# Performance work log

Hardware: AMD Instinct MI355X
Metric: run time of the kernel (lower is better)

The kernel has to match this reference:

```python
import jax, jax.numpy as jnp
import numpy as np

N_WORDS = 256
N_BOOKS = 8
L_WORD = 32
GUMBEL_TEMP = 0.5
EPS_LOG = 1e-9
EPS_GUMBEL = 1e-20


def setup_inputs() -> dict:
    key = jax.random.key(0)
    k1, k2 = jax.random.split(key)
    X = jax.random.normal(k1, (32768, N_BOOKS * L_WORD), dtype=jnp.float32)
    C = jax.random.normal(k2, (N_WORDS, N_BOOKS * L_WORD), dtype=jnp.float32)
    return {"X": X, "C": C}


def reference(X, C):
    N = X.shape[0]
    # (N, B, L) and (M, B, L) per-book views
    x = X.reshape(N, N_BOOKS, L_WORD)
    c = C.reshape(N_WORDS, N_BOOKS, L_WORD)

    xc = jnp.einsum('nbl,mbl->bnm', x, c)            # (B, N, M)
    x2 = jnp.sum(x * x, axis=-1).T[:, :, None]       # (B, N, 1)
    c2 = jnp.sum(c * c, axis=-1).T[:, None, :]       # (B, 1, M)
    logits = 2.0 * xc - x2 - c2                      # (B, N, M)

    # gumbel_softmax sampling path (hard=False): softmax -> log -> +gumbel -> softmax/temp
    p = jax.nn.softmax(logits, axis=-1)
    logp = jnp.log(p + EPS_LOG)
    u = jax.random.uniform(jax.random.key(42), logp.shape, dtype=logp.dtype)
    g = -jnp.log(-jnp.log(u + EPS_GUMBEL) + EPS_GUMBEL)
    soft_prob = jax.nn.softmax((logp + g) / GUMBEL_TEMP, axis=-1)  # (B, N, M)

    # per-book codebook matmul, concatenated along feature dim
    Q = jnp.einsum('bnm,mbl->nbl', soft_prob, c).reshape(N, N_BOOKS * L_WORD)
    return (Q, soft_prob)
```

## Files before the change

kernel.cpp:

```cpp
#include <hip/hip_runtime.h>
#include <stdint.h>

#define NROWS 32768
#define NMQ   (NROWS * 256)
#define QSIZE (NROWS * 256)

typedef __attribute__((ext_vector_type(8))) short short8;
typedef __attribute__((ext_vector_type(4))) float f32x4;

#define LOG2E 1.4426950408889634f

__device__ __forceinline__ uint32_t tfp32(uint32_t idx) {
    const uint32_t K1 = 42u;
    const uint32_t K2 = 0x1BD11BDAu ^ 42u;
    uint32_t x0 = 0u;
    uint32_t x1 = idx + K1;
#define TFR(r) { x0 += x1; x1 = __builtin_rotateleft32(x1, (r)) ^ x0; }
    TFR(13) TFR(15) TFR(26) TFR(6)
    x0 += K1; x1 += K2 + 1u;
    TFR(17) TFR(29) TFR(16) TFR(24)
    x0 += K2; x1 += 2u;
    TFR(13) TFR(15) TFR(26) TFR(6)
    x1 += K1 + 3u;
    TFR(17) TFR(29) TFR(16) TFR(24)
    x0 += K1; x1 += K2 + 4u;
    TFR(13) TFR(15) TFR(26) TFR(6)
    x0 += K2; x1 += 5u;
#undef TFR
    return x0 ^ x1;
}

__device__ __forceinline__ float u01f(uint32_t b) {
    return __uint_as_float((b >> 9) | 0x3F800000u) - 1.0f;
}

__device__ __forceinline__ void split8(const float* p, short8& h, short8& l) {
#pragma unroll
    for (int e = 0; e < 8; ++e) {
        float f = p[e];
        uint32_t ib = __float_as_uint(f);
        h[e] = (short)(ib >> 16);
        float fh = __uint_as_float(ib & 0xFFFF0000u);
        l[e] = (short)(__float_as_uint(f - fh) >> 16);
    }
}

__device__ __forceinline__ unsigned short bf16rne(float f) {
    uint32_t ib = __float_as_uint(f);
    uint32_t r = ib + 0x7FFFu + ((ib >> 16) & 1u);
    return (unsigned short)(r >> 16);
}

#define DPPX(x, ctrl) \
    __int_as_float(__builtin_amdgcn_update_dpp(__float_as_int(x), \
        __float_as_int(x), (ctrl), 0xf, 0xf, false))

__device__ __forceinline__ float red16_max(float x) {
    x = fmaxf(x, DPPX(x, 0xB1));
    x = fmaxf(x, DPPX(x, 0x4E));
    x = fmaxf(x, DPPX(x, 0x141));
    x = fmaxf(x, DPPX(x, 0x140));
    return x;
}
__device__ __forceinline__ float red16_sum(float x) {
    x += DPPX(x, 0xB1);
    x += DPPX(x, 0x4E);
    x += DPPX(x, 0x141);
    x += DPPX(x, 0x140);
    return x;
}

__global__ __launch_bounds__(512)
void pq_fused(const float* __restrict__ X, const float* __restrict__ C,
              float* __restrict__ out)
{
    __shared__ short8 CBH[16 * 64];
    __shared__ short8 CBL[16 * 64];
    __shared__ short8 CQB[16 * 64];
    __shared__ __align__(16) unsigned short PL[8][16][256];
    __shared__ float  C2T[256];

    const int t    = threadIdx.x;
    const int wv   = t >> 6;
    const int lane = t & 63;
    const int g    = lane >> 4;
    const int c    = lane & 15;
    const int b      = blockIdx.x & 7;
    const int rowblk = blockIdx.x >> 3;

    for (int i = t; i < 1024; i += 512) {
        const int tile = i >> 6, l = i & 63;
        const int m = tile * 16 + (l & 15);
        const int kb = (l >> 4) * 8;
        const float* cp = C + (size_t)m * 256 + b * 32 + kb;
        float buf[8];
        *reinterpret_cast<float4*>(&buf[0]) = *reinterpret_cast<const float4*>(cp);
        *reinterpret_cast<float4*>(&buf[4]) = *reinterpret_cast<const float4*>(cp + 4);
        short8 h, lo;
        split8(buf, h, lo);
        CBH[i] = h;
        CBL[i] = lo;
    }
    for (int i = t; i < 1024; i += 512) {
        const int ch = i >> 7, lt = (i >> 6) & 1, l = i & 63;
        const int gg = l >> 4, cc = l & 15;
        short8 v;
#pragma unroll
        for (int e = 0; e < 8; ++e)
            v[e] = (short)bf16rne(C[(size_t)(ch * 32 + gg * 8 + e) * 256 + b * 32 + lt * 16 + cc]);
        CQB[i] = v;
    }
    if (t < 256) {
        const float* cp = C + (size_t)t * 256 + b * 32;
        float s = 0.f;
#pragma unroll
        for (int q = 0; q < 8; ++q) {
            float4 v = *reinterpret_cast<const float4*>(cp + q * 4);
            s = fmaf(v.x, v.x, fmaf(v.y, v.y, fmaf(v.z, v.z, fmaf(v.w, v.w, s))));
        }
        C2T[t] = s;
    }
    __syncthreads();

    float bias[16];
#pragma unroll
    for (int tt = 0; tt < 16; ++tt)
        bias[tt] = -2.0f * LOG2E * C2T[tt * 16 + c];

    float* __restrict__ Qout = out;
    float* __restrict__ SP   = out + QSIZE;

    for (int it = 0; it < 2; ++it) {
        const int r0 = (rowblk << 8) + (it << 7) + (wv << 4);

        short8 xh, xl;
        {
            const float* xp = X + (size_t)(r0 + c) * 256 + b * 32 + g * 8;
            float buf[8];
            *reinterpret_cast<float4*>(&buf[0]) = *reinterpret_cast<const float4*>(xp);
            *reinterpret_cast<float4*>(&buf[4]) = *reinterpret_cast<const float4*>(xp + 4);
            split8(buf, xh, xl);
        }

        f32x4 acc[16];
#pragma unroll
        for (int tt = 0; tt < 16; ++tt) {
            short8 bh = CBH[tt * 64 + lane];
            short8 bl = CBL[tt * 64 + lane];
            f32x4 a = {0.f, 0.f, 0.f, 0.f};
            a = __builtin_amdgcn_mfma_f32_16x16x32_bf16(xh, bh, a, 0, 0, 0);
            a = __builtin_amdgcn_mfma_f32_16x16x32_bf16(xl, bh, a, 0, 0, 0);
            a = __builtin_amdgcn_mfma_f32_16x16x32_bf16(xh, bl, a, 0, 0, 0);
            acc[tt] = a;
        }

#define PROCJ(jj)                                                               \
        {                                                                       \
            const int n = r0 + g * 4 + (jj);                                    \
            const uint32_t base = (uint32_t)b * (uint32_t)NMQ                   \
                                + (uint32_t)n * 256u + (uint32_t)c;             \
            float z[16];                                                        \
            float mx = -3.4e38f;                                                \
            _Pragma("unroll")                                                   \
            for (int tt = 0; tt < 16; ++tt) {                                   \
                uint32_t rb = tfp32(base + (uint32_t)(tt * 16));                \
                float u  = u01f(rb);                                            \
                float tg = -__log2f(u + 1e-20f);                                \
                float lt2 = __log2f(tg);                                        \
                float zz = fmaf(acc[tt][(jj)], 4.0f * LOG2E, bias[tt])          \
                         - 2.0f * lt2;                                          \
                z[tt] = zz;                                                     \
                mx = fmaxf(mx, zz);                                             \
            }                                                                   \
            mx = red16_max(mx);                                                 \
            float s = 0.f;                                                      \
            _Pragma("unroll")                                                   \
            for (int tt = 0; tt < 16; ++tt) {                                   \
                float e = __builtin_amdgcn_exp2f(z[tt] - mx);                   \
                z[tt] = e;                                                      \
                s += e;                                                         \
            }                                                                   \
            s = red16_sum(s);                                                   \
            const float rs = __builtin_amdgcn_rcpf(s);                          \
            float* spg = SP + (size_t)b * NMQ + (size_t)n * 256 + c;            \
            unsigned short* plrow = &PL[wv][g * 4 + (jj)][0];                   \
            _Pragma("unroll")                                                   \
            for (int tt = 0; tt < 16; ++tt) {                                   \
                float p = z[tt] * rs;                                           \
                __builtin_nontemporal_store(p, spg + tt * 16);                  \
                plrow[((tt ^ g) << 4) + c] =                                    \
                    (unsigned short)(__float_as_uint(p) >> 16);                 \
            }                                                                   \
        }
        PROCJ(0) PROCJ(1) PROCJ(2) PROCJ(3)
#undef PROCJ

        {
            f32x4 q0 = {0.f, 0.f, 0.f, 0.f};
            f32x4 q1 = {0.f, 0.f, 0.f, 0.f};
#pragma unroll
            for (int ch = 0; ch < 8; ++ch) {
                const int ttp = (2 * ch + (g >> 1)) ^ (c >> 2);
                const short8 pa = *reinterpret_cast<const short8*>(
                    &PL[wv][c][ttp * 16 + (g & 1) * 8]);
                q0 = __builtin_amdgcn_mfma_f32_16x16x32_bf16(pa, CQB[(ch * 2 + 0) * 64 + lane], q0, 0, 0, 0);
                q1 = __builtin_amdgcn_mfma_f32_16x16x32_bf16(pa, CQB[(ch * 2 + 1) * 64 + lane], q1, 0, 0, 0);
            }
#pragma unroll
            for (int j2 = 0; j2 < 4; ++j2) {
                float* qp = Qout + (size_t)(r0 + g * 4 + j2) * 256 + b * 32 + c;
                __builtin_nontemporal_store(q0[j2], qp);
                __builtin_nontemporal_store(q1[j2], qp + 16);
            }
        }
    }
}

extern "C" void kernel_launch(void* const* d_in, const int* in_sizes, int n_in,
                              void* d_out, int out_size, void* d_ws, size_t ws_size,
                              hipStream_t stream) {
    const float* X = (const float*)d_in[0];
    const float* C = (const float*)d_in[1];
    float* out = (float*)d_out;

    dim3 grid(1024);
    dim3 block(512);
    hipLaunchKernelGGL(pq_fused, grid, block, 0, stream, X, C, out);
}
```

Baseline: 188.4 us.

## Halve probability LDS staging buffer and split Q matmul into two chunks

The per-wave bf16 probability staging buffer shrinks from 16 to 8 rows by running the Q MFMA after every two row-groups instead of once after all four. The C2T scratch array now aliases that buffer, with an extra barrier after the bias load. Launch bounds request 4 blocks per SM so more blocks fit in LDS and registers at once, for better latency hiding. In exchange the Q MFMAs run twice as often, with half the lanes storing redundant rows masked out, so MFMA work doubles.

```diff
diff --git a/kernel.cpp b/kernel.cpp
--- a/kernel.cpp
+++ b/kernel.cpp
@@ -70,15 +70,15 @@
     return x;
 }
 
-__global__ __launch_bounds__(512)
+__global__ __launch_bounds__(512, 4)
 void pq_fused(const float* __restrict__ X, const float* __restrict__ C,
               float* __restrict__ out)
 {
     __shared__ short8 CBH[16 * 64];
     __shared__ short8 CBL[16 * 64];
     __shared__ short8 CQB[16 * 64];
-    __shared__ __align__(16) unsigned short PL[8][16][256];
-    __shared__ float  C2T[256];
+    __shared__ __align__(16) unsigned short PL[8][8][256];
+    float* C2T = reinterpret_cast<float*>(&PL[0][0][0]);
 
     const int t    = threadIdx.x;
     const int wv   = t >> 6;
@@ -126,6 +126,7 @@
 #pragma unroll
     for (int tt = 0; tt < 16; ++tt)
         bias[tt] = -2.0f * LOG2E * C2T[tt * 16 + c];
+    __syncthreads();
 
     float* __restrict__ Qout = out;
     float* __restrict__ SP   = out + QSIZE;
@@ -183,7 +184,7 @@
             s = red16_sum(s);                                                   \
             const float rs = __builtin_amdgcn_rcpf(s);                          \
             float* spg = SP + (size_t)b * NMQ + (size_t)n * 256 + c;            \
-            unsigned short* plrow = &PL[wv][g * 4 + (jj)][0];                   \
+            unsigned short* plrow = &PL[wv][g * 2 + ((jj) & 1)][0];             \
             _Pragma("unroll")                                                   \
             for (int tt = 0; tt < 16; ++tt) {                                   \
                 float p = z[tt] * rs;                                           \
@@ -192,27 +193,37 @@
                     (unsigned short)(__float_as_uint(p) >> 16);                 \
             }                                                                   \
         }
-        PROCJ(0) PROCJ(1) PROCJ(2) PROCJ(3)
+
+#define QCHUNK(joff)                                                            \
+        {                                                                       \
+            f32x4 q0 = {0.f, 0.f, 0.f, 0.f};                                    \
+            f32x4 q1 = {0.f, 0.f, 0.f, 0.f};                                    \
+            _Pragma("unroll")                                                   \
+            for (int ch = 0; ch < 8; ++ch) {                                    \
+                const int ttp = (ch * 2 + (g >> 1)) ^ ((c & 7) >> 1);           \
+                const short8 pa = *reinterpret_cast<const short8*>(             \
+                    &PL[wv][c & 7][ttp * 16 + (g & 1) * 8]);                    \
+                q0 = __builtin_amdgcn_mfma_f32_16x16x32_bf16(                   \
+                         pa, CQB[(ch * 2 + 0) * 64 + lane], q0, 0, 0, 0);       \
+                q1 = __builtin_amdgcn_mfma_f32_16x16x32_bf16(                   \
+                         pa, CQB[(ch * 2 + 1) * 64 + lane], q1, 0, 0, 0);       \
+            }                                                                   \
+            if (g < 2) {                                                        \
+                _Pragma("unroll")                                               \
+                for (int reg = 0; reg < 4; ++reg) {                             \
+                    const int rl = g * 4 + reg;                                 \
+                    const int n = r0 + ((rl >> 1) << 2) + (rl & 1) + (joff);    \
+                    float* qp = Qout + (size_t)n * 256 + b * 32 + c;            \
+                    __builtin_nontemporal_store(q0[reg], qp);                   \
+                    __builtin_nontemporal_store(q1[reg], qp + 16);              \
+                }                                                               \
+            }                                                                   \
+        }
+
+        PROCJ(0) PROCJ(1) QCHUNK(0)
+        PROCJ(2) PROCJ(3) QCHUNK(2)
 #undef PROCJ
-
-        {
-            f32x4 q0 = {0.f, 0.f, 0.f, 0.f};
-            f32x4 q1 = {0.f, 0.f, 0.f, 0.f};
-#pragma unroll
-            for (int ch = 0; ch < 8; ++ch) {
-                const int ttp = (2 * ch + (g >> 1)) ^ (c >> 2);
-                const short8 pa = *reinterpret_cast<const short8*>(
-                    &PL[wv][c][ttp * 16 + (g & 1) * 8]);
-                q0 = __builtin_amdgcn_mfma_f32_16x16x32_bf16(pa, CQB[(ch * 2 + 0) * 64 + lane], q0, 0, 0, 0);
-                q1 = __builtin_amdgcn_mfma_f32_16x16x32_bf16(pa, CQB[(ch * 2 + 1) * 64 + lane], q1, 0, 0, 0);
-            }
-#pragma unroll
-            for (int j2 = 0; j2 < 4; ++j2) {
-                float* qp = Qout + (size_t)(r0 + g * 4 + j2) * 256 + b * 32 + c;
-                __builtin_nontemporal_store(q0[j2], qp);
-                __builtin_nontemporal_store(q1[j2], qp + 16);
-            }
-        }
+#undef QCHUNK
     }
 }
 
```

New measurement: 156.7 us. 16.8% less time.
